# Optimization experiments

Measured on AMD Instinct MI355X. Metric: run time of the kernel, lower is better.

Reference implementation:

```python
import jax, jax.numpy as jnp
import numpy as np

B, S, D, H = 4, 1024, 1024, 16
HS = D // H  # head_size = 64


def setup_inputs() -> dict:
    key = jax.random.key(0)
    ks = jax.random.split(key, 12)
    sc_d = 1.0 / np.sqrt(D)
    sc_h = 1.0 / np.sqrt(HS)
    inp = {
        "queries": jax.random.normal(ks[0], (B, S, D), jnp.float32),
        "keys": jax.random.normal(ks[1], (B, S, D), jnp.float32),
        "values": jax.random.normal(ks[2], (B, S, D), jnp.float32),
        # causal mask: scores where mask == 0 are filled with -1e9
        "mask": jnp.tril(jnp.ones((S, S), jnp.int32)),
        # per-head query/key projections: [H, D, HS] weights, [H, HS] biases
        "Wq": jax.random.uniform(ks[3], (H, D, HS), jnp.float32, -sc_d, sc_d),
        "bq": jax.random.uniform(ks[4], (H, HS), jnp.float32, -sc_d, sc_d),
        "Wk": jax.random.uniform(ks[5], (H, D, HS), jnp.float32, -sc_d, sc_d),
        "bk": jax.random.uniform(ks[6], (H, HS), jnp.float32, -sc_d, sc_d),
        # shared value projection: [D, HS]
        "Wv": jax.random.uniform(ks[7], (D, HS), jnp.float32, -sc_d, sc_d),
        "bv": jax.random.uniform(ks[8], (HS,), jnp.float32, -sc_d, sc_d),
        # output projection: [HS, D]
        "Wo": jax.random.uniform(ks[9], (HS, D), jnp.float32, -sc_h, sc_h),
        "bo": jax.random.uniform(ks[10], (D,), jnp.float32, -sc_h, sc_h),
    }
    return inp


def reference(queries, keys, values, mask, Wq, bq, Wk, bk, Wv, bv, Wo, bo):
    # shared value projection: [B, S, HS]
    v = jnp.einsum("bsd,de->bse", values, Wv) + bv
    # batched per-head projections (replaces the python loop over heads)
    q = jnp.einsum("bsd,hde->bhse", queries, Wq) + bq[None, :, None, :]
    k = jnp.einsum("btd,hde->bhte", keys, Wk) + bk[None, :, None, :]
    scores = jnp.einsum("bhse,bhte->bhst", q, k) / jnp.sqrt(jnp.float32(HS))
    scores = jnp.where(mask == 0, jnp.float32(-1e9), scores)
    attn = jax.nn.softmax(scores, axis=-1)  # [B, H, S, S]; dropout = eval-mode identity
    head_out = jnp.einsum("bhst,bte->bhse", attn, v)
    out = head_out.mean(axis=1)  # mean over heads -> [B, S, HS]
    out = jnp.einsum("bse,ed->bsd", out, Wo) + bo
    attention_weights = attn.mean(axis=1)  # [B, S, S]
    return out, attention_weights
```

## Files before the change

kernel.cpp:

```cpp
#include <hip/hip_runtime.h>
#include <hip/hip_bf16.h>
#include <stdint.h>

typedef _Float16 half8 __attribute__((ext_vector_type(8)));
typedef _Float16 half4 __attribute__((ext_vector_type(4)));
typedef float    f32x4 __attribute__((ext_vector_type(4)));

#define MFMA16(a, b, c) __builtin_amdgcn_mfma_f32_16x16x32_f16(a, b, c, 0, 0, 0)

__global__ __launch_bounds__(256) void transpose_to_f16(
    const float* __restrict__ X, _Float16* __restrict__ Y,
    int R, int C, long inBS, long outBS)
{
    __shared__ float t[32][33];
    const int bz = blockIdx.z;
    X += (long)bz * inBS;
    Y += (long)bz * outBS;
    const int c0 = blockIdx.x * 32, r0 = blockIdx.y * 32;
    const int tx = threadIdx.x & 31, ty = threadIdx.x >> 5;
#pragma unroll
    for (int i = 0; i < 4; ++i)
        t[ty + i * 8][tx] = X[(long)(r0 + ty + i * 8) * C + c0 + tx];
    __syncthreads();
#pragma unroll
    for (int i = 0; i < 4; ++i)
        Y[(long)(c0 + ty + i * 8) * R + r0 + tx] = (_Float16)t[tx][ty + i * 8];
}

__global__ __launch_bounds__(256, 2) void gemm_f16_v2(
    const float* __restrict__ A0, const float* __restrict__ A1,
    const _Float16* __restrict__ BT,
    const float* __restrict__ bias0, const float* __restrict__ bias1,
    void* __restrict__ Cout,
    int N, int lda, int ldbt, int ldc,
    long aBS, long bBS, long cBS,
    int c_half, int atomic, int nks, int kchunk)
{
    __shared__ __align__(16) _Float16 As[128][72];
    __shared__ __align__(16) _Float16 Bs[128][72];

    const int nt = blockIdx.x, mt = blockIdx.y;
    const int b = blockIdx.z / nks, ks = blockIdx.z % nks;
    const int kbeg = ks * kchunk;

    const float* A = A1 ? (b ? A1 : A0) : (A0 + (long)b * aBS);
    const _Float16* Bb = BT + (long)b * bBS;

    const int n0 = nt * 128;
    const int m0 = mt * 128;
    const int tid  = threadIdx.x;
    const int wave = tid >> 6, lane = tid & 63;
    const int m16  = lane & 15, quad = lane >> 4;

    f32x4 acc[2][8];
    {
        f32x4 z = {0.f, 0.f, 0.f, 0.f};
#pragma unroll
        for (int i = 0; i < 2; ++i)
#pragma unroll
            for (int j = 0; j < 8; ++j) acc[i][j] = z;
    }

    for (int k0 = kbeg; k0 < kbeg + kchunk; k0 += 64) {
        {
            const int cc = (tid & 15) * 4;
            const int rb = tid >> 4;
            float4 av[8];
#pragma unroll
            for (int p = 0; p < 8; ++p)
                av[p] = *(const float4*)(A + (long)(m0 + rb + p * 16) * lda + k0 + cc);
#pragma unroll
            for (int p = 0; p < 8; ++p) {
                half4 hv;
                hv[0] = (_Float16)av[p].x; hv[1] = (_Float16)av[p].y;
                hv[2] = (_Float16)av[p].z; hv[3] = (_Float16)av[p].w;
                *(half4*)&As[rb + p * 16][cc] = hv;
            }
        }
        {
            const int j  = tid >> 1;
            const int cc = (tid & 1) * 32;
            int jn = n0 + j; if (jn > N - 1) jn = N - 1;
            const _Float16* bp = Bb + (long)jn * ldbt + k0 + cc;
            half8 b0 = *(const half8*)(bp);
            half8 b1 = *(const half8*)(bp + 8);
            half8 b2 = *(const half8*)(bp + 16);
            half8 b3 = *(const half8*)(bp + 24);
            *(half8*)&Bs[j][cc]      = b0;
            *(half8*)&Bs[j][cc + 8]  = b1;
            *(half8*)&Bs[j][cc + 16] = b2;
            *(half8*)&Bs[j][cc + 24] = b3;
        }
        __syncthreads();
#pragma unroll
        for (int kss = 0; kss < 2; ++kss) {
            const int ko = kss * 32 + quad * 8;
            const half8 a0 = *(const half8*)&As[wave * 32 + m16][ko];
            const half8 a1 = *(const half8*)&As[wave * 32 + 16 + m16][ko];
#pragma unroll
            for (int c = 0; c < 8; ++c) {
                const half8 bf = *(const half8*)&Bs[c * 16 + m16][ko];
                acc[0][c] = MFMA16(a0, bf, acc[0][c]);
                acc[1][c] = MFMA16(a1, bf, acc[1][c]);
            }
        }
        __syncthreads();
    }

    const float* bias = b ? bias1 : bias0;
    const int addb = (bias != nullptr) && (kbeg == 0);
#pragma unroll
    for (int hh = 0; hh < 2; ++hh) {
#pragma unroll
        for (int c = 0; c < 8; ++c) {
            const int col = n0 + c * 16 + m16;
            if (col >= N) continue;
            const float bb = addb ? bias[col] : 0.f;
#pragma unroll
            for (int r = 0; r < 4; ++r) {
                const int row = m0 + wave * 32 + hh * 16 + quad * 4 + r;
                const float v = acc[hh][c][r] + bb;
                const long idx = (long)b * cBS + (long)row * ldc + col;
                if (atomic)      atomicAdd(&((float*)Cout)[idx], v);
                else if (c_half) ((_Float16*)Cout)[idx] = (_Float16)v;
                else             ((float*)Cout)[idx] = v;
            }
        }
    }
}

__global__ __launch_bounds__(256, 2) void attn_stats(
    const _Float16* __restrict__ q_all, const _Float16* __restrict__ k_all,
    float* __restrict__ m_out, float* __restrict__ il_out)
{
    const int st = blockIdx.x, h = blockIdx.y, b = blockIdx.z;
    const int tid = threadIdx.x, wave = tid >> 6, lane = tid & 63;
    const int m16 = lane & 15, quad = lane >> 4;
    const int s0 = st * 64;
    const int sw = s0 + wave * 16;

    __shared__ __align__(16) _Float16 qs[64][72];
    __shared__ __align__(16) _Float16 ks[64][72];

    const int srow = tid >> 2;
    const int scol = (tid & 3) * 16;

    {
        const _Float16* qsrc = q_all + ((long)(b * 1024 + s0 + srow)) * 1024 + h * 64 + scol;
        *(half8*)&qs[srow][scol]     = *(const half8*)(qsrc);
        *(half8*)&qs[srow][scol + 8] = *(const half8*)(qsrc + 8);
    }

    const _Float16* ksrcb = k_all + ((long)(b * 1024 + srow)) * 1024 + h * 64 + scol;

    float mr[4], lr[4];
#pragma unroll
    for (int r = 0; r < 4; ++r) { mr[r] = -3.0e38f; lr[r] = 0.f; }

    half8 a0, a1;
    for (int tt = 0; tt <= st; ++tt) {
        const _Float16* ksrc = ksrcb + (long)(tt * 64) * 1024;
        const half8 k0 = *(const half8*)(ksrc);
        const half8 k1 = *(const half8*)(ksrc + 8);

        __syncthreads();
        *(half8*)&ks[srow][scol]     = k0;
        *(half8*)&ks[srow][scol + 8] = k1;
        __syncthreads();

        if (tt == 0) {
            a0 = *(const half8*)&qs[wave * 16 + m16][quad * 8];
            a1 = *(const half8*)&qs[wave * 16 + m16][quad * 8 + 32];
        }

        if (tt < st) {
#pragma unroll
            for (int c = 0; c < 4; ++c) {
                const half8 b0 = *(const half8*)&ks[c * 16 + m16][quad * 8];
                const half8 b1 = *(const half8*)&ks[c * 16 + m16][quad * 8 + 32];
                f32x4 cc = {0.f, 0.f, 0.f, 0.f};
                cc = MFMA16(a0, b0, cc);
                cc = MFMA16(a1, b1, cc);
#pragma unroll
                for (int r = 0; r < 4; ++r) {
                    const float z  = cc[r] * 0.125f;
                    const float nm = fmaxf(mr[r], z);
                    lr[r] = lr[r] * __expf(mr[r] - nm) + __expf(z - nm);
                    mr[r] = nm;
                }
            }
        } else {
#pragma unroll
            for (int c = 0; c < 4; ++c) {
                const half8 b0 = *(const half8*)&ks[c * 16 + m16][quad * 8];
                const half8 b1 = *(const half8*)&ks[c * 16 + m16][quad * 8 + 32];
                f32x4 cc = {0.f, 0.f, 0.f, 0.f};
                cc = MFMA16(a0, b0, cc);
                cc = MFMA16(a1, b1, cc);
                const int col = tt * 64 + c * 16 + m16;
#pragma unroll
                for (int r = 0; r < 4; ++r) {
                    const int row = sw + quad * 4 + r;
                    if (col <= row) {
                        const float z  = cc[r] * 0.125f;
                        const float nm = fmaxf(mr[r], z);
                        lr[r] = lr[r] * __expf(mr[r] - nm) + __expf(z - nm);
                        mr[r] = nm;
                    }
                }
            }
        }
    }

#pragma unroll
    for (int mk = 1; mk < 16; mk <<= 1) {
#pragma unroll
        for (int r = 0; r < 4; ++r) {
            const float om = __shfl_xor(mr[r], mk);
            const float ol = __shfl_xor(lr[r], mk);
            const float nm = fmaxf(mr[r], om);
            lr[r] = lr[r] * __expf(mr[r] - nm) + ol * __expf(om - nm);
            mr[r] = nm;
        }
    }
    if (m16 == 0) {
#pragma unroll
        for (int r = 0; r < 4; ++r) {
            const long idx = ((long)(b * 16 + h)) * 1024 + sw + quad * 4 + r;
            m_out[idx]  = mr[r];
            il_out[idx] = 1.f / lr[r];
        }
    }
}

__global__ __launch_bounds__(256, 2) void attn_pmean(
    const _Float16* __restrict__ q_all, const _Float16* __restrict__ k_all,
    const float* __restrict__ m_in, const float* __restrict__ il_in,
    float* __restrict__ attn)
{
    const int ttile = blockIdx.x, stile = blockIdx.y, b = blockIdx.z;
    const int tid = threadIdx.x;
    if (ttile > stile) {
        const int c4 = (tid & 15) * 4;
        float4 z = {0.f, 0.f, 0.f, 0.f};
#pragma unroll
        for (int i = 0; i < 4; ++i) {
            const int r = stile * 64 + (tid >> 4) + i * 16;
            *(float4*)&attn[((long)(b * 1024 + r)) * 1024 + ttile * 64 + c4] = z;
        }
        return;
    }

    __shared__ __align__(16) _Float16 qs[64][72];
    __shared__ __align__(16) _Float16 ks[64][72];

    const int wave = tid >> 6, lane = tid & 63;
    const int m16 = lane & 15, quad = lane >> 4;
    const int s0 = stile * 64;
    const int t0 = ttile * 64;
    const int sw = s0 + wave * 16;
    const int diag = (ttile == stile);

    const int srow = tid >> 2;
    const int scol = (tid & 3) * 16;

    const _Float16* qsrc = q_all + ((long)(b * 1024 + s0 + srow)) * 1024 + scol;
    const _Float16* ksrc = k_all + ((long)(b * 1024 + t0 + srow)) * 1024 + scol;
    const long sbase = ((long)(b * 16)) * 1024 + sw + quad * 4;

    float pm[4][4];
#pragma unroll
    for (int c = 0; c < 4; ++c)
#pragma unroll
        for (int r = 0; r < 4; ++r) pm[c][r] = 0.f;

    for (int h = 0; h < 16; ++h) {
        const int ho = h * 64;
        const half8 q0 = *(const half8*)(qsrc + ho);
        const half8 q1 = *(const half8*)(qsrc + ho + 8);
        const half8 k0 = *(const half8*)(ksrc + ho);
        const half8 k1 = *(const half8*)(ksrc + ho + 8);
        const long idx = sbase + (long)h * 1024;
        const float4 mv = *(const float4*)&m_in[idx];
        const float4 iv = *(const float4*)&il_in[idx];

        __syncthreads();
        *(half8*)&qs[srow][scol]     = q0;
        *(half8*)&qs[srow][scol + 8] = q1;
        *(half8*)&ks[srow][scol]     = k0;
        *(half8*)&ks[srow][scol + 8] = k1;
        __syncthreads();

        const half8 a0 = *(const half8*)&qs[wave * 16 + m16][quad * 8];
        const half8 a1 = *(const half8*)&qs[wave * 16 + m16][quad * 8 + 32];
        const float mrow[4] = {mv.x, mv.y, mv.z, mv.w};
        const float irow[4] = {iv.x, iv.y, iv.z, iv.w};

        if (!diag) {
#pragma unroll
            for (int c = 0; c < 4; ++c) {
                const half8 b0 = *(const half8*)&ks[c * 16 + m16][quad * 8];
                const half8 b1 = *(const half8*)&ks[c * 16 + m16][quad * 8 + 32];
                f32x4 cc = {0.f, 0.f, 0.f, 0.f};
                cc = MFMA16(a0, b0, cc);
                cc = MFMA16(a1, b1, cc);
#pragma unroll
                for (int r = 0; r < 4; ++r)
                    pm[c][r] += __expf(cc[r] * 0.125f - mrow[r]) * irow[r];
            }
        } else {
#pragma unroll
            for (int c = 0; c < 4; ++c) {
                const half8 b0 = *(const half8*)&ks[c * 16 + m16][quad * 8];
                const half8 b1 = *(const half8*)&ks[c * 16 + m16][quad * 8 + 32];
                f32x4 cc = {0.f, 0.f, 0.f, 0.f};
                cc = MFMA16(a0, b0, cc);
                cc = MFMA16(a1, b1, cc);
                const int col = t0 + c * 16 + m16;
#pragma unroll
                for (int r = 0; r < 4; ++r) {
                    const int row = sw + quad * 4 + r;
                    if (col <= row)
                        pm[c][r] += __expf(cc[r] * 0.125f - mrow[r]) * irow[r];
                }
            }
        }
    }

#pragma unroll
    for (int c = 0; c < 4; ++c) {
#pragma unroll
        for (int r = 0; r < 4; ++r) {
            const int row = sw + quad * 4 + r;
            const int col = t0 + c * 16 + m16;
            attn[((long)(b * 1024 + row)) * 1024 + col] = pm[c][r] * 0.0625f;
        }
    }
}

extern "C" void kernel_launch(void* const* d_in, const int* in_sizes, int n_in,
                              void* d_out, int out_size, void* d_ws, size_t ws_size,
                              hipStream_t stream)
{
    const float* queries = (const float*)d_in[0];
    const float* keys    = (const float*)d_in[1];
    const float* values  = (const float*)d_in[2];
    const float* Wq = (const float*)d_in[4];
    const float* bq = (const float*)d_in[5];
    const float* Wk = (const float*)d_in[6];
    const float* bk = (const float*)d_in[7];
    const float* Wv = (const float*)d_in[8];
    const float* bv = (const float*)d_in[9];
    const float* Wo = (const float*)d_in[10];
    const float* bo = (const float*)d_in[11];

    float* out_ptr  = (float*)d_out;
    float* attn_ptr = out_ptr + (long)4096 * 1024;

    uint8_t* w = (uint8_t*)d_ws;
    size_t off = 0;
    auto alloc = [&](size_t bytes) {
        void* p = w + off;
        off = (off + bytes + 255) & ~(size_t)255;
        return p;
    };
    _Float16* WqkT  = (_Float16*)alloc((size_t)2 * 1024 * 1024 * 2);
    _Float16* WvT   = (_Float16*)alloc((size_t)64 * 1024 * 2);
    _Float16* WoT   = (_Float16*)alloc((size_t)1024 * 64 * 2);
    _Float16* qkall = (_Float16*)alloc((size_t)2 * 4194304 * 2);
    float*    vbuf  = (float*)alloc((size_t)4096 * 64 * 4);
    _Float16* vT    = (_Float16*)alloc((size_t)4 * 64 * 1024 * 2);
    float*    ctx   = (float*)alloc((size_t)4096 * 64 * 4);
    float*    mbuf  = (float*)alloc((size_t)65536 * 4);
    float*    ilbuf = (float*)alloc((size_t)65536 * 4);
    (void)ws_size; (void)in_sizes; (void)n_in; (void)out_size;

    _Float16* qall = qkall;
    _Float16* kall = qkall + (long)4194304;

    transpose_to_f16<<<dim3(2, 32, 16), 256, 0, stream>>>(Wq, WqkT, 1024, 64, 65536, 65536);
    transpose_to_f16<<<dim3(2, 32, 16), 256, 0, stream>>>(Wk, WqkT + (long)1024 * 1024, 1024, 64, 65536, 65536);
    transpose_to_f16<<<dim3(2, 32, 1),  256, 0, stream>>>(Wv, WvT, 1024, 64, 0, 0);
    transpose_to_f16<<<dim3(32, 2, 1),  256, 0, stream>>>(Wo, WoT, 64, 1024, 0, 0);

    gemm_f16_v2<<<dim3(8, 32, 2), 256, 0, stream>>>(
        queries, keys, WqkT, bq, bk, qkall,
        1024, 1024, 1024, 1024,
        0, (long)1048576, (long)4194304,
        1, 0, 1, 1024);

    hipMemsetAsync(vbuf, 0, (size_t)4096 * 64 * 4, stream);
    gemm_f16_v2<<<dim3(1, 32, 8), 256, 0, stream>>>(
        values, nullptr, WvT, bv, nullptr, vbuf,
        64, 1024, 1024, 64,
        0, 0, 0,
        0, 1, 8, 128);

    transpose_to_f16<<<dim3(2, 32, 4), 256, 0, stream>>>(vbuf, vT, 1024, 64, 65536, 65536);

    attn_stats<<<dim3(16, 16, 4), 256, 0, stream>>>(qall, kall, mbuf, ilbuf);
    attn_pmean<<<dim3(16, 16, 4), 256, 0, stream>>>(qall, kall, mbuf, ilbuf, attn_ptr);

    hipMemsetAsync(ctx, 0, (size_t)4096 * 64 * 4, stream);
    gemm_f16_v2<<<dim3(1, 8, 32), 256, 0, stream>>>(
        attn_ptr, nullptr, vT, nullptr, nullptr, ctx,
        64, 1024, 1024, 64,
        (long)1048576, (long)65536, (long)65536,
        0, 1, 8, 128);

    gemm_f16_v2<<<dim3(8, 32, 1), 256, 0, stream>>>(
        ctx, nullptr, WoT, bo, nullptr, out_ptr,
        1024, 64, 64, 1024,
        0, 0, 0,
        0, 0, 1, 64);
}
```

Baseline: 272.2 us.

## Prefetch next GEMM tile into registers and swizzle workgroups across XCDs

The GEMM main loop now issues the global loads for the next K tile into registers before doing the MFMA work on the current tile, so global memory latency overlaps with compute. Workgroup IDs are also remapped so that consecutive tiles land on the same XCD, which is meant to improve L2 reuse on the multi-die MI355X. The cost is extra live registers for the prefetched A and B fragments, which may lower occupancy under launch_bounds(256,2).

```diff
diff --git a/kernel.cpp b/kernel.cpp
--- a/kernel.cpp
+++ b/kernel.cpp
@@ -39,9 +39,20 @@
     __shared__ __align__(16) _Float16 As[128][72];
     __shared__ __align__(16) _Float16 Bs[128][72];
 
-    const int nt = blockIdx.x, mt = blockIdx.y;
-    const int b = blockIdx.z / nks, ks = blockIdx.z % nks;
+    const int gx  = gridDim.x, gy = gridDim.y;
+    const int nwg = gx * gy * (int)gridDim.z;
+    const int lid = (int)blockIdx.x + gx * ((int)blockIdx.y + gy * (int)blockIdx.z);
+    const int q8  = nwg >> 3, r8 = nwg & 7;
+    const int xcd = lid & 7, loc = lid >> 3;
+    const int sw  = (xcd < r8 ? xcd * (q8 + 1) : r8 * (q8 + 1) + (xcd - r8) * q8) + loc;
+    const int nt  = sw % gx;
+    const int tm2 = sw / gx;
+    const int mt  = tm2 % gy;
+    const int bz  = tm2 / gy;
+
+    const int b = bz / nks, ks = bz % nks;
     const int kbeg = ks * kchunk;
+    const int kend = kbeg + kchunk;
 
     const float* A = A1 ? (b ? A1 : A0) : (A0 + (long)b * aBS);
     const _Float16* Bb = BT + (long)b * bBS;
@@ -52,6 +63,13 @@
     const int wave = tid >> 6, lane = tid & 63;
     const int m16  = lane & 15, quad = lane >> 4;
 
+    const int acol = (tid & 15) * 4;
+    const int arb  = tid >> 4;
+    const int bj   = tid >> 1;
+    const int bcc  = (tid & 1) * 32;
+    int jn = n0 + bj; if (jn > N - 1) jn = N - 1;
+    const _Float16* bpB = Bb + (long)jn * ldbt;
+
     f32x4 acc[2][8];
     {
         f32x4 z = {0.f, 0.f, 0.f, 0.f};
@@ -61,37 +79,38 @@
             for (int j = 0; j < 8; ++j) acc[i][j] = z;
     }
 
-    for (int k0 = kbeg; k0 < kbeg + kchunk; k0 += 64) {
-        {
-            const int cc = (tid & 15) * 4;
-            const int rb = tid >> 4;
-            float4 av[8];
-#pragma unroll
-            for (int p = 0; p < 8; ++p)
-                av[p] = *(const float4*)(A + (long)(m0 + rb + p * 16) * lda + k0 + cc);
-#pragma unroll
-            for (int p = 0; p < 8; ++p) {
-                half4 hv;
-                hv[0] = (_Float16)av[p].x; hv[1] = (_Float16)av[p].y;
-                hv[2] = (_Float16)av[p].z; hv[3] = (_Float16)av[p].w;
-                *(half4*)&As[rb + p * 16][cc] = hv;
-            }
-        }
-        {
-            const int j  = tid >> 1;
-            const int cc = (tid & 1) * 32;
-            int jn = n0 + j; if (jn > N - 1) jn = N - 1;
-            const _Float16* bp = Bb + (long)jn * ldbt + k0 + cc;
-            half8 b0 = *(const half8*)(bp);
-            half8 b1 = *(const half8*)(bp + 8);
-            half8 b2 = *(const half8*)(bp + 16);
-            half8 b3 = *(const half8*)(bp + 24);
-            *(half8*)&Bs[j][cc]      = b0;
-            *(half8*)&Bs[j][cc + 8]  = b1;
-            *(half8*)&Bs[j][cc + 16] = b2;
-            *(half8*)&Bs[j][cc + 24] = b3;
-        }
-        __syncthreads();
+    float4 av[8];
+    half8  bv0, bv1, bv2, bv3;
+
+    auto LOADT = [&](int k0) {
+#pragma unroll
+        for (int p = 0; p < 8; ++p)
+            av[p] = *(const float4*)(A + (long)(m0 + arb + p * 16) * lda + k0 + acol);
+        const _Float16* bp = bpB + k0 + bcc;
+        bv0 = *(const half8*)(bp);
+        bv1 = *(const half8*)(bp + 8);
+        bv2 = *(const half8*)(bp + 16);
+        bv3 = *(const half8*)(bp + 24);
+    };
+    auto STORE_LDS = [&]() {
+#pragma unroll
+        for (int p = 0; p < 8; ++p) {
+            half4 hv;
+            hv[0] = (_Float16)av[p].x; hv[1] = (_Float16)av[p].y;
+            hv[2] = (_Float16)av[p].z; hv[3] = (_Float16)av[p].w;
+            *(half4*)&As[arb + p * 16][acol] = hv;
+        }
+        *(half8*)&Bs[bj][bcc]      = bv0;
+        *(half8*)&Bs[bj][bcc + 8]  = bv1;
+        *(half8*)&Bs[bj][bcc + 16] = bv2;
+        *(half8*)&Bs[bj][bcc + 24] = bv3;
+    };
+
+    LOADT(kbeg);
+    for (int k0 = kbeg; k0 < kend; k0 += 64) {
+        STORE_LDS();
+        __syncthreads();
+        if (k0 + 64 < kend) LOADT(k0 + 64);
 #pragma unroll
         for (int kss = 0; kss < 2; ++kss) {
             const int ko = kss * 32 + quad * 8;
```

New measurement: 251.7 us. -7.5%, faster.
